# Performance work log

Hardware: AMD Instinct MI355X
Metric: run time of the kernel (lower is better)

## Reference

```python
import jax, jax.numpy as jnp
from jax import lax
import numpy as np

# Problem dims (from init_kwargs / input_specs)
B, NC, NX, NY = 16, 31, 256, 256   # cube: batch, spectral channels, spatial
NO, KX, KY = 3, 17, 17             # diffraction orders, kernel spatial size
PAD = 4                            # findclusters dilation padding
N_LOC = NO * NC * (2 * PAD + 1) ** 2  # 7533 trainable kernel entries


def _build_locations():
    """Emulate findclusters: one dispersion delta per (order, channel),
    dilated by a (2*PAD+1)^2 window. Returns flat int32 indices into
    the flattened (NO, NC, KX, KY) kernel."""
    idxs = []
    cy = KX // 2  # 8
    lo, hi = PAD, KX - 1 - PAD  # valid center range [4, 12]
    for o in range(NO):
        for c in range(NC):
            # channel-dependent horizontal dispersion, order-dependent sign
            shift = (o - 1) * (c * PAD * 2 // (NC - 1))
            cx = int(np.clip(cy + shift, lo, hi))
            for dy in range(-PAD, PAD + 1):
                for dx in range(-PAD, PAD + 1):
                    idxs.append(((o * NC + c) * KX + (cy + dy)) * KY + (cx + dx))
    return jnp.asarray(np.array(idxs, dtype=np.int32))


def setup_inputs() -> dict:
    key = jax.random.key(0)
    k1, k2 = jax.random.split(key)
    x = jax.random.normal(k1, (B, NC, NX, NY), dtype=jnp.float32)
    # trainable sparse kernel values (mostly positive so ReLU passes most)
    variable_kernel = jax.random.uniform(k2, (N_LOC,), dtype=jnp.float32,
                                         minval=-0.2, maxval=1.0)
    locations = _build_locations()
    return {"x": x, "variable_kernel": variable_kernel, "locations": locations}


def reference(x, variable_kernel, locations):
    # fill_kernel: scatter ReLU'd trainable values into a zero kernel
    kernel = (jnp.zeros((NO * NC * KX * KY,), x.dtype)
              .at[locations].set(jax.nn.relu(variable_kernel))
              .reshape(NO, NC, KX, KY))
    # disperse_all_orders: per-order dispersion conv, summed over spectral
    # channels -> measurement per order. out: (B, NO, NX, NY)
    out = lax.conv_general_dilated(
        x, kernel, window_strides=(1, 1), padding="SAME",
        dimension_numbers=("NCHW", "OIHW", "NCHW"))
    return out
```

## Files before the change

### kernel.cpp

```cpp
#include <hip/hip_runtime.h>

namespace {

constexpr int kB  = 16;
constexpr int kNC = 31;
constexpr int kNX = 256;
constexpr int kNY = 256;
constexpr int kNO = 3;
constexpr int kKS = 17;
constexpr int NOC = kNO * kNC;

constexpr int TX = 64;
constexpr int TY = 64;
constexpr int HTY = TY + 8;
constexpr int TCOL = 76;
constexpr int XP   = 80;
constexpr int W12  = 12;

__global__ void prep(const float* __restrict__ vk, const int* __restrict__ loc,
                     float* __restrict__ w12, int* __restrict__ soaTab)
{
    int i = blockIdx.x * 256 + threadIdx.x;
    if (i < NOC * 9 * W12) {
        int row = i / W12;
        int dp  = i - row * W12;
        int oc  = row / 9;
        int so = loc[oc * 81] - (oc * kKS + 4) * kKS;
        int rs = so & 3;
        float v = 0.0f;
        if (dp >= rs && dp < rs + 9) {
            float t = vk[row * 9 + (dp - rs)];
            v = t > 0.0f ? t : 0.0f;
        }
        w12[i] = v;
    }
    if (i < NOC) {
        int so = loc[i * 81] - (i * kKS + 4) * kKS;
        soaTab[i] = so & ~3;
    }
}

__global__ __launch_bounds__(256, 3)
void disperse_conv(const float* __restrict__ x,
                   const float* __restrict__ w12,
                   const int* __restrict__ soaTab,
                   float* __restrict__ out)
{
    __shared__ __align__(16) float xtile[HTY * XP];

    const int tid = threadIdx.x;
    const int x0 = blockIdx.x * TX;
    const int y0 = blockIdx.y * TY;
    const int bz = blockIdx.z;
    const int b  = bz / 3;
    const int o  = bz - 3 * b;

    const int tx = tid & 15;
    const int ty = tid >> 4;
    const int xo = tx * 4;

    float acc[4][4];
    #pragma unroll
    for (int jr = 0; jr < 4; ++jr)
        #pragma unroll
        for (int jj = 0; jj < 4; ++jj)
            acc[jr][jj] = 0.0f;

    for (int c = 0; c < kNC; ++c) {
        const int soa = soaTab[o * kNC + c];
        const float* wch = w12 + (size_t)((o * kNC + c) * 9) * W12;
        const float* xc  = x + (size_t)(b * kNC + c) * kNX * kNY;

        __syncthreads();
        #pragma unroll
        for (int it = 0; it < 6; ++it) {
            int i = it * 256 + tid;
            if (i < HTY * 19) {
                int r  = i / 19;
                int mc = i - r * 19;
                int gy = y0 - 4 + r;
                int gx = x0 + soa - 8 + mc * 4;
                float4 v = make_float4(0.f, 0.f, 0.f, 0.f);
                if ((unsigned)gy < (unsigned)kNX && (unsigned)gx < (unsigned)kNY)
                    v = *(const float4*)(xc + (size_t)gy * kNY + gx);
                *(float4*)&xtile[r * XP + mc * 4] = v;
            }
        }
        __syncthreads();

        #pragma unroll
        for (int m = 0; m < 12; ++m) {
            const int row = ty * 4 + m;
            const float* p = &xtile[row * XP + xo];
            const float4 q0 = *(const float4*)(p);
            const float4 q1 = *(const float4*)(p + 4);
            const float4 q2 = *(const float4*)(p + 8);
            const float4 q3 = *(const float4*)(p + 12);
            const float xr[16] = { q0.x, q0.y, q0.z, q0.w,
                                   q1.x, q1.y, q1.z, q1.w,
                                   q2.x, q2.y, q2.z, q2.w,
                                   q3.x, q3.y, q3.z, q3.w };

            #pragma unroll
            for (int jr = 0; jr < 4; ++jr) {
                const int dy = m - jr;
                if (dy < 0 || dy >= 9) continue;
                const float* wr = wch + dy * W12;
                const float4 wa = *(const float4*)(wr);
                const float4 wb = *(const float4*)(wr + 4);
                const float4 wc = *(const float4*)(wr + 8);

                #pragma unroll
                for (int jj = 0; jj < 4; ++jj) {
                    float a = acc[jr][jj];
                    a = fmaf(wa.x, xr[jj + 0], a);
                    a = fmaf(wa.y, xr[jj + 1], a);
                    a = fmaf(wa.z, xr[jj + 2], a);
                    a = fmaf(wa.w, xr[jj + 3], a);
                    a = fmaf(wb.x, xr[jj + 4], a);
                    a = fmaf(wb.y, xr[jj + 5], a);
                    a = fmaf(wb.z, xr[jj + 6], a);
                    a = fmaf(wb.w, xr[jj + 7], a);
                    a = fmaf(wc.x, xr[jj + 8], a);
                    a = fmaf(wc.y, xr[jj + 9], a);
                    a = fmaf(wc.z, xr[jj + 10], a);
                    a = fmaf(wc.w, xr[jj + 11], a);
                    acc[jr][jj] = a;
                }
            }
        }
    }

    #pragma unroll
    for (int jr = 0; jr < 4; ++jr) {
        size_t base = (((size_t)b * kNO + o) * kNX + (size_t)(y0 + ty * 4 + jr)) * kNY
                      + (size_t)(x0 + xo);
        *(float4*)(out + base) = make_float4(acc[jr][0], acc[jr][1],
                                             acc[jr][2], acc[jr][3]);
    }
}

}

extern "C" void kernel_launch(void* const* d_in, const int* in_sizes, int n_in,
                              void* d_out, int out_size, void* d_ws, size_t ws_size,
                              hipStream_t stream)
{
    const float* x  = (const float*)d_in[0];
    const float* vk = (const float*)d_in[1];
    const int* loc  = (const int*)d_in[2];
    float* outp = (float*)d_out;

    float* w12 = (float*)d_ws;
    int*   soaTab = (int*)(w12 + NOC * 9 * W12);

    dim3 pgrid((NOC * 9 * W12 + 255) / 256);
    hipLaunchKernelGGL(prep, pgrid, dim3(256), 0, stream, vk, loc, w12, soaTab);

    dim3 grid(kNY / TX, kNX / TY, kB * kNO);
    hipLaunchKernelGGL(disperse_conv, grid, dim3(256), 0, stream,
                       x, w12, soaTab, outp);
}
```

Measured before the change: 447.9 us.

## Double-buffer shared x tile with register prefetch of next channel

Splits the shared-memory input tile into two buffers. The global loads for channel c+1 are issued into registers before the FMA loop for channel c and written to the other buffer afterwards, so load latency overlaps compute and each channel needs one barrier instead of two. The tile row/column index math is also precomputed once per thread. The cost is doubled LDS per block and 24 extra live registers, which may cut occupancy below the 3-blocks-per-CU launch bound or cause spills.

```diff
diff --git a/kernel.cpp b/kernel.cpp
--- a/kernel.cpp
+++ b/kernel.cpp
@@ -10,12 +10,13 @@
 constexpr int kKS = 17;
 constexpr int NOC = kNO * kNC;
 
-constexpr int TX = 64;
-constexpr int TY = 64;
+constexpr int TX  = 64;
+constexpr int TY  = 64;
 constexpr int HTY = TY + 8;
-constexpr int TCOL = 76;
-constexpr int XP   = 80;
-constexpr int W12  = 12;
+constexpr int NF4 = 19;
+constexpr int XP  = 80;
+constexpr int W12 = 12;
+constexpr int NSTG = HTY * NF4;
 
 __global__ void prep(const float* __restrict__ vk, const int* __restrict__ loc,
                      float* __restrict__ w12, int* __restrict__ soaTab)
@@ -25,8 +26,8 @@
         int row = i / W12;
         int dp  = i - row * W12;
         int oc  = row / 9;
-        int so = loc[oc * 81] - (oc * kKS + 4) * kKS;
-        int rs = so & 3;
+        int so  = loc[oc * 81] - (oc * kKS + 4) * kKS;
+        int rs  = so & 3;
         float v = 0.0f;
         if (dp >= rs && dp < rs + 9) {
             float t = vk[row * 9 + (dp - rs)];
@@ -46,7 +47,7 @@
                    const int* __restrict__ soaTab,
                    float* __restrict__ out)
 {
-    __shared__ __align__(16) float xtile[HTY * XP];
+    __shared__ __align__(16) float xt[2][HTY * XP];
 
     const int tid = threadIdx.x;
     const int x0 = blockIdx.x * TX;
@@ -59,6 +60,32 @@
     const int ty = tid >> 4;
     const int xo = tx * 4;
 
+    int sr[6], sm[6];
+    #pragma unroll
+    for (int it = 0; it < 6; ++it) {
+        int i = it * 256 + tid;
+        sr[it] = i / NF4;
+        sm[it] = i - NF4 * sr[it];
+    }
+
+    {
+        const int soa = soaTab[o * kNC];
+        const float* xc = x + (size_t)(b * kNC) * kNX * kNY;
+        #pragma unroll
+        for (int it = 0; it < 6; ++it) {
+            int i = it * 256 + tid;
+            if (i < NSTG) {
+                int gy  = y0 - 4 + sr[it];
+                int gxa = x0 + soa - 8 + sm[it] * 4;
+                float4 v = make_float4(0.f, 0.f, 0.f, 0.f);
+                if ((unsigned)gy < (unsigned)kNX && (unsigned)gxa < (unsigned)kNY)
+                    v = *(const float4*)(xc + (size_t)gy * kNY + gxa);
+                *(float4*)&xt[0][sr[it] * XP + sm[it] * 4] = v;
+            }
+        }
+    }
+    __syncthreads();
+
     float acc[4][4];
     #pragma unroll
     for (int jr = 0; jr < 4; ++jr)
@@ -67,35 +94,38 @@
             acc[jr][jj] = 0.0f;
 
     for (int c = 0; c < kNC; ++c) {
-        const int soa = soaTab[o * kNC + c];
+        float4 p0 = make_float4(0.f, 0.f, 0.f, 0.f);
+        float4 p1 = p0, p2 = p0, p3 = p0, p4 = p0, p5 = p0;
+        const bool pfv = (c + 1 < kNC);
+        if (pfv) {
+            const int soa1 = soaTab[o * kNC + c + 1];
+            const float* xc1 = x + (size_t)(b * kNC + c + 1) * kNX * kNY;
+            int gy, gxa;
+            gy = y0 - 4 + sr[0]; gxa = x0 + soa1 - 8 + sm[0] * 4;
+            if ((unsigned)gy < 256u && (unsigned)gxa < 256u) p0 = *(const float4*)(xc1 + (size_t)gy * kNY + gxa);
+            gy = y0 - 4 + sr[1]; gxa = x0 + soa1 - 8 + sm[1] * 4;
+            if ((unsigned)gy < 256u && (unsigned)gxa < 256u) p1 = *(const float4*)(xc1 + (size_t)gy * kNY + gxa);
+            gy = y0 - 4 + sr[2]; gxa = x0 + soa1 - 8 + sm[2] * 4;
+            if ((unsigned)gy < 256u && (unsigned)gxa < 256u) p2 = *(const float4*)(xc1 + (size_t)gy * kNY + gxa);
+            gy = y0 - 4 + sr[3]; gxa = x0 + soa1 - 8 + sm[3] * 4;
+            if ((unsigned)gy < 256u && (unsigned)gxa < 256u) p3 = *(const float4*)(xc1 + (size_t)gy * kNY + gxa);
+            gy = y0 - 4 + sr[4]; gxa = x0 + soa1 - 8 + sm[4] * 4;
+            if ((unsigned)gy < 256u && (unsigned)gxa < 256u) p4 = *(const float4*)(xc1 + (size_t)gy * kNY + gxa);
+            if (tid < NSTG - 1280) {
+                gy = y0 - 4 + sr[5]; gxa = x0 + soa1 - 8 + sm[5] * 4;
+                if ((unsigned)gy < 256u && (unsigned)gxa < 256u) p5 = *(const float4*)(xc1 + (size_t)gy * kNY + gxa);
+            }
+        }
+
+        const float* buf = &xt[c & 1][0];
         const float* wch = w12 + (size_t)((o * kNC + c) * 9) * W12;
-        const float* xc  = x + (size_t)(b * kNC + c) * kNX * kNY;
-
-        __syncthreads();
-        #pragma unroll
-        for (int it = 0; it < 6; ++it) {
-            int i = it * 256 + tid;
-            if (i < HTY * 19) {
-                int r  = i / 19;
-                int mc = i - r * 19;
-                int gy = y0 - 4 + r;
-                int gx = x0 + soa - 8 + mc * 4;
-                float4 v = make_float4(0.f, 0.f, 0.f, 0.f);
-                if ((unsigned)gy < (unsigned)kNX && (unsigned)gx < (unsigned)kNY)
-                    v = *(const float4*)(xc + (size_t)gy * kNY + gx);
-                *(float4*)&xtile[r * XP + mc * 4] = v;
-            }
-        }
-        __syncthreads();
-
         #pragma unroll
         for (int m = 0; m < 12; ++m) {
-            const int row = ty * 4 + m;
-            const float* p = &xtile[row * XP + xo];
-            const float4 q0 = *(const float4*)(p);
-            const float4 q1 = *(const float4*)(p + 4);
-            const float4 q2 = *(const float4*)(p + 8);
-            const float4 q3 = *(const float4*)(p + 12);
+            const float* pp = &buf[(ty * 4 + m) * XP + xo];
+            const float4 q0 = *(const float4*)(pp);
+            const float4 q1 = *(const float4*)(pp + 4);
+            const float4 q2 = *(const float4*)(pp + 8);
+            const float4 q3 = *(const float4*)(pp + 12);
             const float xr[16] = { q0.x, q0.y, q0.z, q0.w,
                                    q1.x, q1.y, q1.z, q1.w,
                                    q2.x, q2.y, q2.z, q2.w,
@@ -129,6 +159,18 @@
                 }
             }
         }
+
+        if (pfv) {
+            float* dst = &xt[(c + 1) & 1][0];
+            *(float4*)&dst[sr[0] * XP + sm[0] * 4] = p0;
+            *(float4*)&dst[sr[1] * XP + sm[1] * 4] = p1;
+            *(float4*)&dst[sr[2] * XP + sm[2] * 4] = p2;
+            *(float4*)&dst[sr[3] * XP + sm[3] * 4] = p3;
+            *(float4*)&dst[sr[4] * XP + sm[4] * 4] = p4;
+            if (tid < NSTG - 1280)
+                *(float4*)&dst[sr[5] * XP + sm[5] * 4] = p5;
+        }
+        __syncthreads();
     }
 
     #pragma unroll
```

Result: slower. 1.616 ms (+260.9%).

## Split channel reduction across two blocks and combine with atomic adds

Applied to the files above, without the earlier changes.

Splits the 31-channel reduction into two halves, so each (batch, order) tile is handled by two blocks, doubling the grid. Partial sums are combined with float atomicAdd into an output zeroed by a memset, and the launch-bounds occupancy hint goes from 3 to 6. The goal is more parallelism and occupancy on the 256-CU device, whose base grid of 768 blocks does not fill it well. In exchange it adds a memset, atomic traffic, and non-deterministic summation order.

```diff
diff --git a/kernel.cpp b/kernel.cpp
--- a/kernel.cpp
+++ b/kernel.cpp
@@ -10,12 +10,13 @@
 constexpr int kKS = 17;
 constexpr int NOC = kNO * kNC;
 
-constexpr int TX = 64;
-constexpr int TY = 64;
+constexpr int TX  = 64;
+constexpr int TY  = 64;
 constexpr int HTY = TY + 8;
-constexpr int TCOL = 76;
-constexpr int XP   = 80;
-constexpr int W12  = 12;
+constexpr int NF4 = 19;
+constexpr int XP  = 80;
+constexpr int W12 = 12;
+constexpr int NSPL = 2;
 
 __global__ void prep(const float* __restrict__ vk, const int* __restrict__ loc,
                      float* __restrict__ w12, int* __restrict__ soaTab)
@@ -25,8 +26,8 @@
         int row = i / W12;
         int dp  = i - row * W12;
         int oc  = row / 9;
-        int so = loc[oc * 81] - (oc * kKS + 4) * kKS;
-        int rs = so & 3;
+        int so  = loc[oc * 81] - (oc * kKS + 4) * kKS;
+        int rs  = so & 3;
         float v = 0.0f;
         if (dp >= rs && dp < rs + 9) {
             float t = vk[row * 9 + (dp - rs)];
@@ -40,7 +41,7 @@
     }
 }
 
-__global__ __launch_bounds__(256, 3)
+__global__ __launch_bounds__(256, 6)
 void disperse_conv(const float* __restrict__ x,
                    const float* __restrict__ w12,
                    const int* __restrict__ soaTab,
@@ -52,8 +53,12 @@
     const int x0 = blockIdx.x * TX;
     const int y0 = blockIdx.y * TY;
     const int bz = blockIdx.z;
-    const int b  = bz / 3;
-    const int o  = bz - 3 * b;
+    const int b  = bz / 6;
+    const int r6 = bz - 6 * b;
+    const int o  = r6 >> 1;
+    const int s  = r6 & 1;
+    const int cbeg = s ? 16 : 0;
+    const int cend = s ? kNC : 16;
 
     const int tx = tid & 15;
     const int ty = tid >> 4;
@@ -66,7 +71,7 @@
         for (int jj = 0; jj < 4; ++jj)
             acc[jr][jj] = 0.0f;
 
-    for (int c = 0; c < kNC; ++c) {
+    for (int c = cbeg; c < cend; ++c) {
         const int soa = soaTab[o * kNC + c];
         const float* wch = w12 + (size_t)((o * kNC + c) * 9) * W12;
         const float* xc  = x + (size_t)(b * kNC + c) * kNX * kNY;
@@ -75,27 +80,26 @@
         #pragma unroll
         for (int it = 0; it < 6; ++it) {
             int i = it * 256 + tid;
-            if (i < HTY * 19) {
-                int r  = i / 19;
-                int mc = i - r * 19;
-                int gy = y0 - 4 + r;
+            if (i < HTY * NF4) {
+                int rr = i / NF4;
+                int mc = i - rr * NF4;
+                int gy = y0 - 4 + rr;
                 int gx = x0 + soa - 8 + mc * 4;
                 float4 v = make_float4(0.f, 0.f, 0.f, 0.f);
                 if ((unsigned)gy < (unsigned)kNX && (unsigned)gx < (unsigned)kNY)
                     v = *(const float4*)(xc + (size_t)gy * kNY + gx);
-                *(float4*)&xtile[r * XP + mc * 4] = v;
+                *(float4*)&xtile[rr * XP + mc * 4] = v;
             }
         }
         __syncthreads();
 
         #pragma unroll
         for (int m = 0; m < 12; ++m) {
-            const int row = ty * 4 + m;
-            const float* p = &xtile[row * XP + xo];
-            const float4 q0 = *(const float4*)(p);
-            const float4 q1 = *(const float4*)(p + 4);
-            const float4 q2 = *(const float4*)(p + 8);
-            const float4 q3 = *(const float4*)(p + 12);
+            const float* pp = &xtile[(ty * 4 + m) * XP + xo];
+            const float4 q0 = *(const float4*)(pp);
+            const float4 q1 = *(const float4*)(pp + 4);
+            const float4 q2 = *(const float4*)(pp + 8);
+            const float4 q3 = *(const float4*)(pp + 12);
             const float xr[16] = { q0.x, q0.y, q0.z, q0.w,
                                    q1.x, q1.y, q1.z, q1.w,
                                    q2.x, q2.y, q2.z, q2.w,
@@ -135,8 +139,9 @@
     for (int jr = 0; jr < 4; ++jr) {
         size_t base = (((size_t)b * kNO + o) * kNX + (size_t)(y0 + ty * 4 + jr)) * kNY
                       + (size_t)(x0 + xo);
-        *(float4*)(out + base) = make_float4(acc[jr][0], acc[jr][1],
-                                             acc[jr][2], acc[jr][3]);
+        #pragma unroll
+        for (int jj = 0; jj < 4; ++jj)
+            atomicAdd(out + base + jj, acc[jr][jj]);
     }
 }
 
@@ -154,10 +159,12 @@
     float* w12 = (float*)d_ws;
     int*   soaTab = (int*)(w12 + NOC * 9 * W12);
 
+    hipMemsetAsync(d_out, 0, (size_t)out_size * sizeof(float), stream);
+
     dim3 pgrid((NOC * 9 * W12 + 255) / 256);
     hipLaunchKernelGGL(prep, pgrid, dim3(256), 0, stream, vk, loc, w12, soaTab);
 
-    dim3 grid(kNY / TX, kNX / TY, kB * kNO);
+    dim3 grid(kNY / TX, kNX / TY, kB * kNO * NSPL);
     hipLaunchKernelGGL(disperse_conv, grid, dim3(256), 0, stream,
                        x, w12, soaTab, outp);
 }
```

After: 468.4 us. 1.05x slower.
